# Optimization experiments

Measured on AMD Instinct MI355X. Metric: run time of the kernel, lower is better.

The kernel has to match this reference:

```python
import jax, jax.numpy as jnp
import numpy as np

H = 24  # num_heads
EPS = 1e-6


def _rmsnorm(t, scale):
    # per-last-dim RMSNorm in fp32, as in the torch RMSNorm
    tf = t.astype(jnp.float32)
    rrms = jax.lax.rsqrt(jnp.mean(tf * tf, axis=-1, keepdims=True) + EPS)
    return (tf * rrms).astype(t.dtype) * scale


def setup_inputs() -> dict:
    key = jax.random.key(0)
    k1, k2, k3 = jax.random.split(key, 3)
    B, L, D = 2, 2048, 3072
    x = jax.random.normal(k1, (B, L, D), dtype=jnp.float32)
    qkv_w = jax.random.normal(k2, (3 * D, D), dtype=jnp.float32) * (1.0 / np.sqrt(D))
    proj_w = jax.random.normal(k3, (D, D), dtype=jnp.float32) * (1.0 / np.sqrt(D))
    q_scale = jnp.ones((D // H,), dtype=jnp.float32)
    k_scale = jnp.ones((D // H,), dtype=jnp.float32)
    return {"x": x, "qkv_w": qkv_w, "q_scale": q_scale, "k_scale": k_scale, "proj_w": proj_w}


def reference(x, qkv_w, q_scale, k_scale, proj_w):
    B, L, D = x.shape
    Hd = D // H
    # fused QKV projection: [B, L, 3D]
    qkv = jnp.einsum("bld,ed->ble", x, qkv_w)
    # split into q, k, v: [B, H, L, Hd] each
    qkv = qkv.reshape(B, L, 3, H, Hd).transpose(2, 0, 3, 1, 4)
    q, k, v = qkv[0], qkv[1], qkv[2]
    # QK RMSNorm (per head_dim), cast back to v dtype
    q = _rmsnorm(q, q_scale).astype(v.dtype)
    k = _rmsnorm(k, k_scale).astype(v.dtype)
    # scaled dot-product attention
    scores = jnp.einsum("bhqd,bhkd->bhqk", q, k) / jnp.sqrt(jnp.asarray(Hd, q.dtype))
    attn = jax.nn.softmax(scores, axis=-1)
    out = jnp.einsum("bhqk,bhkd->bhqd", attn, v)
    # merge heads: [B, L, D]
    out = out.transpose(0, 2, 1, 3).reshape(B, L, D)
    # output projection
    return jnp.einsum("bld,ed->ble", out, proj_w)
```

## Files before the change

kernel.cpp:

```cpp
#include <hip/hip_runtime.h>

typedef unsigned short u16;
typedef unsigned int u32;
typedef __bf16 bf16x8 __attribute__((ext_vector_type(8)));
typedef u16 u16x8 __attribute__((ext_vector_type(8)));
typedef float f32x4 __attribute__((ext_vector_type(4)));

#define NH 24
#define SL 2048
#define DM 3072
#define HD 128
#define NB 2
#define MM (NB*SL)
#define NE (3*DM)

__device__ __forceinline__ float b2f(u16 u) { return __builtin_bit_cast(float, (u32)u << 16); }
__device__ __forceinline__ u16 f2b(float f) {
  u32 x = __builtin_bit_cast(u32, f);
  return (u16)((x + 0x7fffu + ((x >> 16) & 1u)) >> 16);
}
__device__ __forceinline__ float fexp2(float x) {
#if __has_builtin(__builtin_amdgcn_exp2f)
  return __builtin_amdgcn_exp2f(x);
#else
  return exp2f(x);
#endif
}

__device__ __forceinline__ void stage16(const u16* g, u16* l, int lane) {
#if __has_builtin(__builtin_amdgcn_global_load_lds)
  __builtin_amdgcn_global_load_lds((const __attribute__((address_space(1))) void*)g,
                                   (__attribute__((address_space(3))) void*)l, 16, 0, 0);
#else
  reinterpret_cast<u16x8*>(l)[lane] = *reinterpret_cast<const u16x8*>(g);
#endif
}

__device__ __forceinline__ int xcd_swz(int lin, int nwg) {
  int cpx = nwg >> 3;
  return (lin & 7) * cpx + (lin >> 3);
}

__global__ __launch_bounds__(256) void cvt_kernel(const float* __restrict__ src,
                                                  u16* __restrict__ dst, int n4) {
  int i = blockIdx.x * 256 + threadIdx.x;
  if (i >= n4) return;
  float4 v = reinterpret_cast<const float4*>(src)[i];
  u32 lo = (u32)f2b(v.x) | ((u32)f2b(v.y) << 16);
  u32 hi = (u32)f2b(v.z) | ((u32)f2b(v.w) << 16);
  reinterpret_cast<uint2*>(dst)[i] = make_uint2(lo, hi);
}

__global__ __launch_bounds__(256) void gemm_qkv(const u16* __restrict__ A, const u16* __restrict__ Bw,
                                                u16* __restrict__ qb, u16* __restrict__ kb,
                                                u16* __restrict__ vb) {
  __shared__ __align__(16) u16 Asm[128*32];
  __shared__ __align__(16) u16 Bsm[128*32];
  const int tid = threadIdx.x;
  const int w = tid >> 6, lane = tid & 63;
  const int fq = lane >> 4, fr = lane & 15;
  const int wr = w >> 1, wc = w & 1;
  const int nwg = gridDim.x * gridDim.y;
  const int swz = xcd_swz(blockIdx.y * gridDim.x + blockIdx.x, nwg);
  const int m0 = (swz % gridDim.x) * 128;
  const int e0 = (swz / gridDim.x) * 128;
  const int K = DM;
  const int c0 = 2*w, c1 = 2*w + 1;
  const int row0 = lane >> 2;
  const int koff = (lane & 3) * 8;

  f32x4 acc[4][4] = {};

  for (int kt = 0; kt < K; kt += 32) {
    __syncthreads();
    stage16(A + (size_t)(m0 + c0*16 + row0)*K + kt + koff, Asm + c0*512, lane);
    stage16(A + (size_t)(m0 + c1*16 + row0)*K + kt + koff, Asm + c1*512, lane);
    stage16(Bw + (size_t)(e0 + c0*16 + row0)*K + kt + koff, Bsm + c0*512, lane);
    stage16(Bw + (size_t)(e0 + c1*16 + row0)*K + kt + koff, Bsm + c1*512, lane);
    __syncthreads();
    bf16x8 af[4], bfr[4];
#pragma unroll
    for (int m = 0; m < 4; ++m)
      af[m] = *reinterpret_cast<const bf16x8*>(Asm + (wr*64 + m*16 + fr)*32 + fq*8);
#pragma unroll
    for (int n = 0; n < 4; ++n)
      bfr[n] = *reinterpret_cast<const bf16x8*>(Bsm + (wc*64 + n*16 + fr)*32 + fq*8);
#pragma unroll
    for (int m = 0; m < 4; ++m)
#pragma unroll
      for (int n = 0; n < 4; ++n)
        acc[m][n] = __builtin_amdgcn_mfma_f32_16x16x32_bf16(af[m], bfr[n], acc[m][n], 0, 0, 0);
  }

  const int s = e0 / DM;
  const int h = (e0 % DM) >> 7;
  const int b = m0 >> 11;
  const int l0 = m0 & (SL - 1);
  u16* outb = (s == 0) ? qb : (s == 1) ? kb : vb;
  outb += ((size_t)(b*NH + h)*SL + l0) * HD;
#pragma unroll
  for (int m = 0; m < 4; ++m)
#pragma unroll
    for (int n = 0; n < 4; ++n)
#pragma unroll
      for (int j = 0; j < 4; ++j) {
        int rr = wr*64 + m*16 + fq*4 + j;
        int cc = wc*64 + n*16 + fr;
        outb[(size_t)rr*HD + cc] = f2b(acc[m][n][j]);
      }
}

__global__ __launch_bounds__(256) void gemm_proj(const u16* __restrict__ A, const u16* __restrict__ Bw,
                                                 float* __restrict__ Y) {
  __shared__ __align__(16) u16 Asm[128*32];
  __shared__ __align__(16) u16 Bsm[128*32];
  const int tid = threadIdx.x;
  const int w = tid >> 6, lane = tid & 63;
  const int fq = lane >> 4, fr = lane & 15;
  const int wr = w >> 1, wc = w & 1;
  const int nwg = gridDim.x * gridDim.y;
  const int swz = xcd_swz(blockIdx.y * gridDim.x + blockIdx.x, nwg);
  const int m0 = (swz % gridDim.x) * 128;
  const int e0 = (swz / gridDim.x) * 128;
  const int K = DM;
  const int c0 = 2*w, c1 = 2*w + 1;
  const int row0 = lane >> 2;
  const int koff = (lane & 3) * 8;

  f32x4 acc[4][4] = {};

  for (int kt = 0; kt < K; kt += 32) {
    __syncthreads();
    stage16(A + (size_t)(m0 + c0*16 + row0)*K + kt + koff, Asm + c0*512, lane);
    stage16(A + (size_t)(m0 + c1*16 + row0)*K + kt + koff, Asm + c1*512, lane);
    stage16(Bw + (size_t)(e0 + c0*16 + row0)*K + kt + koff, Bsm + c0*512, lane);
    stage16(Bw + (size_t)(e0 + c1*16 + row0)*K + kt + koff, Bsm + c1*512, lane);
    __syncthreads();
    bf16x8 af[4], bfr[4];
#pragma unroll
    for (int m = 0; m < 4; ++m)
      af[m] = *reinterpret_cast<const bf16x8*>(Asm + (wr*64 + m*16 + fr)*32 + fq*8);
#pragma unroll
    for (int n = 0; n < 4; ++n)
      bfr[n] = *reinterpret_cast<const bf16x8*>(Bsm + (wc*64 + n*16 + fr)*32 + fq*8);
#pragma unroll
    for (int m = 0; m < 4; ++m)
#pragma unroll
      for (int n = 0; n < 4; ++n)
        acc[m][n] = __builtin_amdgcn_mfma_f32_16x16x32_bf16(af[m], bfr[n], acc[m][n], 0, 0, 0);
  }

  float* y = Y + (size_t)m0*DM + e0;
#pragma unroll
  for (int m = 0; m < 4; ++m)
#pragma unroll
    for (int n = 0; n < 4; ++n)
#pragma unroll
      for (int j = 0; j < 4; ++j) {
        int rr = wr*64 + m*16 + fq*4 + j;
        int cc = wc*64 + n*16 + fr;
        y[(size_t)rr*DM + cc] = acc[m][n][j];
      }
}

__global__ __launch_bounds__(256) void rmsnorm_k(u16* __restrict__ buf, const float* __restrict__ scale,
                                                 float extra) {
  int row = blockIdx.x * 4 + (threadIdx.x >> 6);
  int lane = threadIdx.x & 63;
  u16* p = buf + (size_t)row * HD + lane * 2;
  u32 u = *reinterpret_cast<const u32*>(p);
  float a = b2f((u16)(u & 0xffffu));
  float c = b2f((u16)(u >> 16));
  float ss = a*a + c*c;
#pragma unroll
  for (int m = 32; m; m >>= 1) ss += __shfl_xor(ss, m, 64);
  float rr = rsqrtf(ss * (1.0f/128.0f) + 1e-6f);
  float s0 = scale[lane*2] * extra;
  float s1 = scale[lane*2 + 1] * extra;
  u32 o = (u32)f2b(a*rr*s0) | ((u32)f2b(c*rr*s1) << 16);
  *reinterpret_cast<u32*>(p) = o;
}

__global__ __launch_bounds__(512) void attn_kernel(const u16* __restrict__ qb, const u16* __restrict__ kb,
                                                   const u16* __restrict__ vb, u16* __restrict__ ob) {
  __shared__ __align__(16) u16 Ksm[64*136];
  __shared__ __align__(16) u16 Vsm[128*72];
  __shared__ __align__(16) u16 Psm[128*72];
  const int tid = threadIdx.x;
  const int w = tid >> 6, lane = tid & 63;
  const int fq = lane >> 4, fr = lane & 15;
  const int bh = blockIdx.y;
  const int q0 = blockIdx.x * 128;
  const u16* qrow = qb + (size_t)bh * SL * HD;
  const u16* krow = kb + (size_t)bh * SL * HD;
  const u16* vrow = vb + (size_t)bh * SL * HD;

  bf16x8 qf[4];
#pragma unroll
  for (int kk = 0; kk < 4; ++kk)
    qf[kk] = *reinterpret_cast<const bf16x8*>(qrow + (size_t)(q0 + w*16 + fr)*HD + kk*32 + fq*8);

  f32x4 o[8] = {};
  float mrow[4], lrow[4];
#pragma unroll
  for (int j = 0; j < 4; ++j) { mrow[j] = -1e30f; lrow[j] = 0.0f; }

  for (int kt = 0; kt < SL; kt += 64) {
    __syncthreads();
    for (int c = tid; c < 1024; c += 512) {
      int key = c >> 4;
      int cc = (c & 15) * 8;
      *reinterpret_cast<bf16x8*>(Ksm + key*136 + cc) =
          *reinterpret_cast<const bf16x8*>(krow + (size_t)(kt + key)*HD + cc);
      u16x8 vv = *reinterpret_cast<const u16x8*>(vrow + (size_t)(kt + key)*HD + cc);
      int skey = key ^ ((cc >> 3) & 7) << 3;
#pragma unroll
      for (int j2 = 0; j2 < 8; ++j2)
        Vsm[(cc + j2)*72 + skey] = vv[j2];
    }
    __syncthreads();

    f32x4 s[4] = {};
#pragma unroll
    for (int kk = 0; kk < 4; ++kk)
#pragma unroll
      for (int n = 0; n < 4; ++n) {
        bf16x8 kf = *reinterpret_cast<const bf16x8*>(Ksm + (n*16 + fr)*136 + kk*32 + fq*8);
        s[n] = __builtin_amdgcn_mfma_f32_16x16x32_bf16(qf[kk], kf, s[n], 0, 0, 0);
      }

    float corr[4];
#pragma unroll
    for (int j = 0; j < 4; ++j) {
      float t = fmaxf(fmaxf(s[0][j], s[1][j]), fmaxf(s[2][j], s[3][j]));
      t = fmaxf(t, __shfl_xor(t, 1, 64));
      t = fmaxf(t, __shfl_xor(t, 2, 64));
      t = fmaxf(t, __shfl_xor(t, 4, 64));
      t = fmaxf(t, __shfl_xor(t, 8, 64));
      float mn = fmaxf(mrow[j], t);
      corr[j] = fexp2(mrow[j] - mn);
      float sum = 0.0f;
#pragma unroll
      for (int n = 0; n < 4; ++n) {
        float pv = fexp2(s[n][j] - mn);
        s[n][j] = pv;
        sum += pv;
      }
      sum += __shfl_xor(sum, 1, 64);
      sum += __shfl_xor(sum, 2, 64);
      sum += __shfl_xor(sum, 4, 64);
      sum += __shfl_xor(sum, 8, 64);
      lrow[j] = lrow[j]*corr[j] + sum;
      mrow[j] = mn;
    }
#pragma unroll
    for (int nn = 0; nn < 8; ++nn)
#pragma unroll
      for (int j = 0; j < 4; ++j)
        o[nn][j] *= corr[j];

#pragma unroll
    for (int n = 0; n < 4; ++n)
#pragma unroll
      for (int j = 0; j < 4; ++j)
        Psm[(w*16 + fq*4 + j)*72 + n*16 + fr] = f2b(s[n][j]);
    __syncthreads();

#pragma unroll
    for (int kk2 = 0; kk2 < 2; ++kk2) {
      bf16x8 pf = *reinterpret_cast<const bf16x8*>(Psm + (w*16 + fr)*72 + kk2*32 + fq*8);
#pragma unroll
      for (int nn = 0; nn < 8; ++nn) {
        int row = nn*16 + fr;
        int xr = ((row >> 3) & 7) << 3;
        bf16x8 vf = *reinterpret_cast<const bf16x8*>(Vsm + row*72 + ((kk2*32 + fq*8) ^ xr));
        o[nn] = __builtin_amdgcn_mfma_f32_16x16x32_bf16(pf, vf, o[nn], 0, 0, 0);
      }
    }
  }

  const int b = bh / NH, h = bh % NH;
  u16* op = ob + (size_t)b * SL * DM + (size_t)h * HD;
#pragma unroll
  for (int nn = 0; nn < 8; ++nn)
#pragma unroll
    for (int j = 0; j < 4; ++j) {
      int r = q0 + w*16 + fq*4 + j;
      op[(size_t)r*DM + nn*16 + fr] = f2b(o[nn][j] / lrow[j]);
    }
}

extern "C" void kernel_launch(void* const* d_in, const int* in_sizes, int n_in,
                              void* d_out, int out_size, void* d_ws, size_t ws_size,
                              hipStream_t stream) {
  const float* x       = (const float*)d_in[0];
  const float* qkv_w   = (const float*)d_in[1];
  const float* q_scale = (const float*)d_in[2];
  const float* k_scale = (const float*)d_in[3];
  const float* proj_w  = (const float*)d_in[4];
  float* y = (float*)d_out;

  u16* regA = (u16*)d_ws;
  u16* regB = regA + (size_t)MM*DM;
  u16* qbuf = regB + (size_t)NE*DM;
  u16* kbuf = qbuf + (size_t)NB*NH*SL*HD;
  u16* vbuf = kbuf + (size_t)NB*NH*SL*HD;

  const int n4x = MM*DM/4, n4w = NE*DM/4, n4p = DM*DM/4;
  cvt_kernel<<<dim3((n4x + 255)/256), 256, 0, stream>>>(x, regA, n4x);
  cvt_kernel<<<dim3((n4w + 255)/256), 256, 0, stream>>>(qkv_w, regB, n4w);

  gemm_qkv<<<dim3(MM/128, NE/128), 256, 0, stream>>>(regA, regB, qbuf, kbuf, vbuf);

  const float QS = 1.4426950408889634f / 11.313708498984761f;
  rmsnorm_k<<<dim3(NB*NH*SL/4), 256, 0, stream>>>(qbuf, q_scale, QS);
  rmsnorm_k<<<dim3(NB*NH*SL/4), 256, 0, stream>>>(kbuf, k_scale, 1.0f);

  cvt_kernel<<<dim3((n4p + 255)/256), 256, 0, stream>>>(proj_w, regB, n4p);

  attn_kernel<<<dim3(SL/128, NB*NH), 512, 0, stream>>>(qbuf, kbuf, vbuf, regA);

  gemm_proj<<<dim3(MM/128, DM/128), 256, 0, stream>>>(regA, regB, y);
}
```

Measured before the change: 902.0 us.

## Rewrite GEMMs with 256x192 tiles, double-buffered LDS and swizzled layout

Both projection GEMMs move from 128x128 single-buffered tiles with 256 threads to 256x192 tiles with 512 threads. The LDS buffers are double-buffered so the next K-slice loads while the current one feeds MFMA, the LDS layout is XOR-swizzled to cut bank conflicts, and setprio/sched barriers interleave MFMA with LDS reads. The goal is more reuse per loaded byte and hiding global-load latency. In exchange it uses more registers and LDS, and the QKV epilogue now splits a 192-wide column block across heads with a per-element head computation.

```diff
diff --git a/kernel.cpp b/kernel.cpp
--- a/kernel.cpp
+++ b/kernel.cpp
@@ -13,6 +13,11 @@
 #define NB 2
 #define MM (NB*SL)
 #define NE (3*DM)
+
+#define BM 256
+#define BN 192
+#define BK 32
+#define NT (DM/BK)
 
 __device__ __forceinline__ float b2f(u16 u) { return __builtin_bit_cast(float, (u32)u << 16); }
 __device__ __forceinline__ u16 f2b(float f) {
@@ -51,115 +56,139 @@
   reinterpret_cast<uint2*>(dst)[i] = make_uint2(lo, hi);
 }
 
-__global__ __launch_bounds__(256) void gemm_qkv(const u16* __restrict__ A, const u16* __restrict__ Bw,
-                                                u16* __restrict__ qb, u16* __restrict__ kb,
-                                                u16* __restrict__ vb) {
-  __shared__ __align__(16) u16 Asm[128*32];
-  __shared__ __align__(16) u16 Bsm[128*32];
+
+#define GEMM_STAGE(Aptr, Bptr, kt, Asd, Bsd)                                          \
+  {                                                                                   \
+    const int r_in = lane >> 2;                                                       \
+    const int gcol = (((lane & 3) ^ (r_in & 3)) << 3);                                \
+    _Pragma("unroll")                                                                 \
+    for (int i = 0; i < 2; ++i) {                                                     \
+      int ch = w + i * 8;                                                             \
+      stage16(Aptr + (size_t)(m0 + ch * 16 + r_in) * DM + (kt) + gcol,                \
+              (Asd) + ch * 512, lane);                                                \
+    }                                                                                 \
+    stage16(Bptr + (size_t)(e0 + w * 16 + r_in) * DM + (kt) + gcol,                   \
+            (Bsd) + w * 512, lane);                                                   \
+    if (w < 4)                                                                        \
+      stage16(Bptr + (size_t)(e0 + (w + 8) * 16 + r_in) * DM + (kt) + gcol,           \
+              (Bsd) + (w + 8) * 512, lane);                                           \
+  }
+
+#define GEMM_KLOOP(Aptr, Bptr)                                                        \
+  f32x4 acc[8][3] = {};                                                               \
+  GEMM_STAGE(Aptr, Bptr, 0, As[0], Bs[0]);                                            \
+  __syncthreads();                                                                    \
+  for (int t = 0; t < NT; ++t) {                                                      \
+    const int c = t & 1;                                                              \
+    const u16* Asc = As[c];                                                           \
+    const u16* Bsc = Bs[c];                                                           \
+    bf16x8 bfr[3], a0[4];                                                             \
+    _Pragma("unroll")                                                                 \
+    for (int n = 0; n < 3; ++n) {                                                     \
+      int row = wc * 48 + n * 16 + fr;                                                \
+      bfr[n] = *reinterpret_cast<const bf16x8*>(Bsc + row * 32 +                      \
+                                                ((fq ^ (row & 3)) << 3));             \
+    }                                                                                 \
+    _Pragma("unroll")                                                                 \
+    for (int m = 0; m < 4; ++m) {                                                     \
+      int row = wr * 128 + m * 16 + fr;                                               \
+      a0[m] = *reinterpret_cast<const bf16x8*>(Asc + row * 32 +                       \
+                                               ((fq ^ (row & 3)) << 3));              \
+    }                                                                                 \
+    if (t + 1 < NT) { GEMM_STAGE(Aptr, Bptr, (t + 1) * BK, As[c ^ 1], Bs[c ^ 1]); }   \
+    __builtin_amdgcn_s_barrier();                                                     \
+    __builtin_amdgcn_sched_barrier(0);                                                \
+    __builtin_amdgcn_s_setprio(1);                                                    \
+    _Pragma("unroll")                                                                 \
+    for (int m = 0; m < 4; ++m)                                                       \
+      _Pragma("unroll")                                                               \
+      for (int n = 0; n < 3; ++n)                                                     \
+        acc[m][n] = __builtin_amdgcn_mfma_f32_16x16x32_bf16(a0[m], bfr[n],            \
+                                                            acc[m][n], 0, 0, 0);     \
+    __builtin_amdgcn_s_setprio(0);                                                    \
+    __builtin_amdgcn_s_barrier();                                                     \
+    __builtin_amdgcn_sched_barrier(0);                                                \
+    _Pragma("unroll")                                                                 \
+    for (int m = 0; m < 4; ++m) {                                                     \
+      int row = wr * 128 + (m + 4) * 16 + fr;                                         \
+      a0[m] = *reinterpret_cast<const bf16x8*>(Asc + row * 32 +                       \
+                                               ((fq ^ (row & 3)) << 3));              \
+    }                                                                                 \
+    __builtin_amdgcn_s_barrier();                                                     \
+    __builtin_amdgcn_sched_barrier(0);                                                \
+    __builtin_amdgcn_s_setprio(1);                                                    \
+    _Pragma("unroll")                                                                 \
+    for (int m = 0; m < 4; ++m)                                                       \
+      _Pragma("unroll")                                                               \
+      for (int n = 0; n < 3; ++n)                                                     \
+        acc[m + 4][n] = __builtin_amdgcn_mfma_f32_16x16x32_bf16(a0[m], bfr[n],        \
+                                                                acc[m + 4][n],       \
+                                                                0, 0, 0);             \
+    __builtin_amdgcn_s_setprio(0);                                                    \
+    __syncthreads();                                                                  \
+  }
+
+__global__ __launch_bounds__(512, 2) void gemm_qkv(const u16* __restrict__ A,
+                                                   const u16* __restrict__ Bw,
+                                                   u16* __restrict__ qb,
+                                                   u16* __restrict__ kb,
+                                                   u16* __restrict__ vb) {
+  __shared__ __align__(16) u16 As[2][BM * BK];
+  __shared__ __align__(16) u16 Bs[2][BN * BK];
   const int tid = threadIdx.x;
   const int w = tid >> 6, lane = tid & 63;
   const int fq = lane >> 4, fr = lane & 15;
-  const int wr = w >> 1, wc = w & 1;
-  const int nwg = gridDim.x * gridDim.y;
-  const int swz = xcd_swz(blockIdx.y * gridDim.x + blockIdx.x, nwg);
-  const int m0 = (swz % gridDim.x) * 128;
-  const int e0 = (swz / gridDim.x) * 128;
-  const int K = DM;
-  const int c0 = 2*w, c1 = 2*w + 1;
-  const int row0 = lane >> 2;
-  const int koff = (lane & 3) * 8;
-
-  f32x4 acc[4][4] = {};
-
-  for (int kt = 0; kt < K; kt += 32) {
-    __syncthreads();
-    stage16(A + (size_t)(m0 + c0*16 + row0)*K + kt + koff, Asm + c0*512, lane);
-    stage16(A + (size_t)(m0 + c1*16 + row0)*K + kt + koff, Asm + c1*512, lane);
-    stage16(Bw + (size_t)(e0 + c0*16 + row0)*K + kt + koff, Bsm + c0*512, lane);
-    stage16(Bw + (size_t)(e0 + c1*16 + row0)*K + kt + koff, Bsm + c1*512, lane);
-    __syncthreads();
-    bf16x8 af[4], bfr[4];
-#pragma unroll
-    for (int m = 0; m < 4; ++m)
-      af[m] = *reinterpret_cast<const bf16x8*>(Asm + (wr*64 + m*16 + fr)*32 + fq*8);
-#pragma unroll
-    for (int n = 0; n < 4; ++n)
-      bfr[n] = *reinterpret_cast<const bf16x8*>(Bsm + (wc*64 + n*16 + fr)*32 + fq*8);
-#pragma unroll
-    for (int m = 0; m < 4; ++m)
-#pragma unroll
-      for (int n = 0; n < 4; ++n)
-        acc[m][n] = __builtin_amdgcn_mfma_f32_16x16x32_bf16(af[m], bfr[n], acc[m][n], 0, 0, 0);
-  }
+  const int wr = w >> 2, wc = w & 3;
+  const int gx = gridDim.x;
+  const int swz = xcd_swz(blockIdx.y * gx + blockIdx.x, gx * gridDim.y);
+  const int m0 = (swz % gx) * BM;
+  const int e0 = (swz / gx) * BN;
+
+  GEMM_KLOOP(A, Bw);
 
   const int s = e0 / DM;
-  const int h = (e0 % DM) >> 7;
+  const int ecol = e0 % DM;
   const int b = m0 >> 11;
   const int l0 = m0 & (SL - 1);
   u16* outb = (s == 0) ? qb : (s == 1) ? kb : vb;
-  outb += ((size_t)(b*NH + h)*SL + l0) * HD;
-#pragma unroll
-  for (int m = 0; m < 4; ++m)
-#pragma unroll
-    for (int n = 0; n < 4; ++n)
+#pragma unroll
+  for (int m = 0; m < 8; ++m)
+#pragma unroll
+    for (int n = 0; n < 3; ++n)
 #pragma unroll
       for (int j = 0; j < 4; ++j) {
-        int rr = wr*64 + m*16 + fq*4 + j;
-        int cc = wc*64 + n*16 + fr;
-        outb[(size_t)rr*HD + cc] = f2b(acc[m][n][j]);
-      }
-}
-
-__global__ __launch_bounds__(256) void gemm_proj(const u16* __restrict__ A, const u16* __restrict__ Bw,
-                                                 float* __restrict__ Y) {
-  __shared__ __align__(16) u16 Asm[128*32];
-  __shared__ __align__(16) u16 Bsm[128*32];
+        int rr = wr * 128 + m * 16 + fq * 4 + j;
+        int cc = ecol + wc * 48 + n * 16 + fr;
+        int h = cc >> 7, d = cc & 127;
+        outb[((size_t)(b * NH + h) * SL + l0 + rr) * HD + d] = f2b(acc[m][n][j]);
+      }
+}
+
+__global__ __launch_bounds__(512, 2) void gemm_proj(const u16* __restrict__ A,
+                                                    const u16* __restrict__ Bw,
+                                                    float* __restrict__ Y) {
+  __shared__ __align__(16) u16 As[2][BM * BK];
+  __shared__ __align__(16) u16 Bs[2][BN * BK];
   const int tid = threadIdx.x;
   const int w = tid >> 6, lane = tid & 63;
   const int fq = lane >> 4, fr = lane & 15;
-  const int wr = w >> 1, wc = w & 1;
-  const int nwg = gridDim.x * gridDim.y;
-  const int swz = xcd_swz(blockIdx.y * gridDim.x + blockIdx.x, nwg);
-  const int m0 = (swz % gridDim.x) * 128;
-  const int e0 = (swz / gridDim.x) * 128;
-  const int K = DM;
-  const int c0 = 2*w, c1 = 2*w + 1;
-  const int row0 = lane >> 2;
-  const int koff = (lane & 3) * 8;
-
-  f32x4 acc[4][4] = {};
-
-  for (int kt = 0; kt < K; kt += 32) {
-    __syncthreads();
-    stage16(A + (size_t)(m0 + c0*16 + row0)*K + kt + koff, Asm + c0*512, lane);
-    stage16(A + (size_t)(m0 + c1*16 + row0)*K + kt + koff, Asm + c1*512, lane);
-    stage16(Bw + (size_t)(e0 + c0*16 + row0)*K + kt + koff, Bsm + c0*512, lane);
-    stage16(Bw + (size_t)(e0 + c1*16 + row0)*K + kt + koff, Bsm + c1*512, lane);
-    __syncthreads();
-    bf16x8 af[4], bfr[4];
-#pragma unroll
-    for (int m = 0; m < 4; ++m)
-      af[m] = *reinterpret_cast<const bf16x8*>(Asm + (wr*64 + m*16 + fr)*32 + fq*8);
-#pragma unroll
-    for (int n = 0; n < 4; ++n)
-      bfr[n] = *reinterpret_cast<const bf16x8*>(Bsm + (wc*64 + n*16 + fr)*32 + fq*8);
-#pragma unroll
-    for (int m = 0; m < 4; ++m)
-#pragma unroll
-      for (int n = 0; n < 4; ++n)
-        acc[m][n] = __builtin_amdgcn_mfma_f32_16x16x32_bf16(af[m], bfr[n], acc[m][n], 0, 0, 0);
-  }
-
-  float* y = Y + (size_t)m0*DM + e0;
-#pragma unroll
-  for (int m = 0; m < 4; ++m)
-#pragma unroll
-    for (int n = 0; n < 4; ++n)
+  const int wr = w >> 2, wc = w & 3;
+  const int gx = gridDim.x;
+  const int swz = xcd_swz(blockIdx.y * gx + blockIdx.x, gx * gridDim.y);
+  const int m0 = (swz % gx) * BM;
+  const int e0 = (swz / gx) * BN;
+
+  GEMM_KLOOP(A, Bw);
+
+#pragma unroll
+  for (int m = 0; m < 8; ++m)
+#pragma unroll
+    for (int n = 0; n < 3; ++n)
 #pragma unroll
       for (int j = 0; j < 4; ++j) {
-        int rr = wr*64 + m*16 + fq*4 + j;
-        int cc = wc*64 + n*16 + fr;
-        y[(size_t)rr*DM + cc] = acc[m][n][j];
+        int rr = wr * 128 + m * 16 + fq * 4 + j;
+        int cc = wc * 48 + n * 16 + fr;
+        Y[(size_t)(m0 + rr) * DM + e0 + cc] = acc[m][n][j];
       }
 }
 
@@ -310,7 +339,7 @@
   cvt_kernel<<<dim3((n4x + 255)/256), 256, 0, stream>>>(x, regA, n4x);
   cvt_kernel<<<dim3((n4w + 255)/256), 256, 0, stream>>>(qkv_w, regB, n4w);
 
-  gemm_qkv<<<dim3(MM/128, NE/128), 256, 0, stream>>>(regA, regB, qbuf, kbuf, vbuf);
+  gemm_qkv<<<dim3(MM/BM, NE/BN), 512, 0, stream>>>(regA, regB, qbuf, kbuf, vbuf);
 
   const float QS = 1.4426950408889634f / 11.313708498984761f;
   rmsnorm_k<<<dim3(NB*NH*SL/4), 256, 0, stream>>>(qbuf, q_scale, QS);
@@ -320,5 +349,5 @@
 
   attn_kernel<<<dim3(SL/128, NB*NH), 512, 0, stream>>>(qbuf, kbuf, vbuf, regA);
 
-  gemm_proj<<<dim3(MM/128, DM/128), 256, 0, stream>>>(regA, regB, y);
-}
+  gemm_proj<<<dim3(MM/BM, DM/BN), 512, 0, stream>>>(regA, regB, y);
+}
```

Result: faster. 867.9 us (-3.8%).
